# Performance work log

Hardware: AMD Instinct MI355X
Metric: run time of the kernel (lower is better)

The kernel has to match this reference:

```python
import jax, jax.numpy as jnp
import numpy as np

H = 16   # num_attention_heads
G = 4    # num_gqa_groups
D = 64   # head_dim = hidden // H
HIDDEN = 1024
KV_DIM = HIDDEN // H * G  # 256
EPS = 1e-5


def setup_inputs() -> dict:
    key = jax.random.key(0)
    k0, k1, k2, k3 = jax.random.split(key, 4)
    x = jax.random.normal(k0, (8, 4096, HIDDEN), dtype=jnp.float32)
    query_weight = jax.random.normal(k1, (HIDDEN, HIDDEN), dtype=jnp.float32) * 0.02
    key_weight = jax.random.normal(k2, (KV_DIM, HIDDEN), dtype=jnp.float32) * 0.02
    value_weight = jax.random.normal(k3, (KV_DIM, HIDDEN), dtype=jnp.float32) * 0.02
    return {
        "x": x,
        "query_weight": query_weight,
        "key_weight": key_weight,
        "value_weight": value_weight,
        "query_bias": jnp.zeros((HIDDEN,), jnp.float32),
        "key_bias": jnp.zeros((KV_DIM,), jnp.float32),
        "value_bias": jnp.zeros((KV_DIM,), jnp.float32),
        "layer_norm_weight": jnp.ones((HIDDEN,), jnp.float32),
        "layer_norm_bias": jnp.zeros((HIDDEN,), jnp.float32),
    }


def reference(x, query_weight, key_weight, value_weight, query_bias, key_bias,
              value_bias, layer_norm_weight, layer_norm_bias):
    b, s, _ = x.shape
    # Shared LayerNorm (q is k is v path in apply_qkv_norm)
    mu = jnp.mean(x, axis=-1, keepdims=True)
    var = jnp.mean(jnp.square(x - mu), axis=-1, keepdims=True)
    xn = (x - mu) * jax.lax.rsqrt(var + EPS) * layer_norm_weight + layer_norm_bias
    # Q/K/V projections (F.linear: x @ W.T + b)
    q = xn @ query_weight.T + query_bias           # [b, s, H*D]
    k = xn @ key_weight.T + key_bias               # [b, s, G*1*D]
    v = xn @ value_weight.T + value_bias           # [b, s, G*1*D]
    # 'b s (h d) -> b h s d'
    q = q.reshape(b, s, H, D).transpose(0, 2, 1, 3)           # [b, H, s, D]
    # 'b s (g h d) -> b h (g s) d' with h = KV_DIM//(G*D) = 1
    def kv_rearrange(t):
        t = t.reshape(b, s, G, 1, D)                          # b s g h d
        t = t.transpose(0, 3, 2, 1, 4)                        # b h g s d
        return t.reshape(b, 1, G * s, D)                      # [b, 1, G*s, D]
    return q, kv_rearrange(k), kv_rearrange(v)
```

## Files before the change

kernel.cpp:

```cpp
#include <hip/hip_runtime.h>
#include <hip/hip_bf16.h>


#define HIDDEN 1024
#define NTOK   32768

typedef __bf16 bf16x8 __attribute__((ext_vector_type(8)));
typedef float  f32x4  __attribute__((ext_vector_type(4)));

#define GLOBAL_AS(p) ((const __attribute__((address_space(1))) void*)(p))
#define LDS_AS(p)    ((__attribute__((address_space(3))) void*)(p))

__device__ __forceinline__ unsigned short f2bf(float f) {
  union { float f; unsigned int i; } x; x.f = f;
  unsigned int r = x.i + 0x7FFFu + ((x.i >> 16) & 1u);
  return (unsigned short)(r >> 16);
}

__global__ __launch_bounds__(256) void ln_kernel(
    const float* __restrict__ x,
    const float* __restrict__ gamma,
    const float* __restrict__ beta,
    unsigned short* __restrict__ xn) {
  const int row = blockIdx.x;
  const int t   = threadIdx.x;
  const size_t base = (size_t)row * HIDDEN;

  const float4 v = ((const float4*)(x + base))[t];
  float s  = v.x + v.y + v.z + v.w;
  float s2 = v.x*v.x + v.y*v.y + v.z*v.z + v.w*v.w;
#pragma unroll
  for (int off = 32; off >= 1; off >>= 1) {
    s  += __shfl_xor(s,  off);
    s2 += __shfl_xor(s2, off);
  }
  __shared__ float red[8];
  const int w = t >> 6;
  if ((t & 63) == 0) { red[w] = s; red[4 + w] = s2; }
  __syncthreads();
  s  = red[0] + red[1] + red[2] + red[3];
  s2 = red[4] + red[5] + red[6] + red[7];
  const float mu   = s * (1.0f / HIDDEN);
  const float rstd = rsqrtf(s2 * (1.0f / HIDDEN) - mu * mu + 1e-5f);

  const float4 g  = ((const float4*)gamma)[t];
  const float4 bb = ((const float4*)beta)[t];
  ushort4 o;
  o.x = f2bf((v.x - mu) * rstd * g.x + bb.x);
  o.y = f2bf((v.y - mu) * rstd * g.y + bb.y);
  o.z = f2bf((v.z - mu) * rstd * g.z + bb.z);
  o.w = f2bf((v.w - mu) * rstd * g.w + bb.w);
  ((ushort4*)(xn + base))[t] = o;
}

__global__ __launch_bounds__(256) void cvt_kernel(
    const float* __restrict__ src, unsigned short* __restrict__ dst) {
  const int i = blockIdx.x * 256 + threadIdx.x;
  const float4 v = ((const float4*)src)[i];
  ushort4 o;
  o.x = f2bf(v.x); o.y = f2bf(v.y); o.z = f2bf(v.z); o.w = f2bf(v.w);
  ((ushort4*)dst)[i] = o;
}

__global__ __launch_bounds__(512, 2) void qkv_gemm(
    const unsigned short* __restrict__ xn,
    const unsigned short* __restrict__ wq,
    const unsigned short* __restrict__ wk,
    const unsigned short* __restrict__ wv,
    const float* __restrict__ bq,
    const float* __restrict__ bk,
    const float* __restrict__ bv,
    float* __restrict__ out) {
  __shared__ unsigned short Al[4 * 8192];
  __shared__ unsigned short Bl[4 * 8192];

  const int bid = blockIdx.x;
  const int swz = (bid & 7) * 96 + (bid >> 3);
  const int mt  = swz / 6;
  const int nt  = swz % 6;
  const int brow = mt * 256;

  const unsigned short* wbase; const float* biasptr;
  int segcol; size_t obase; int hg;
  if (nt < 4)       { wbase = wq + (size_t)nt * 256 * HIDDEN; biasptr = bq; segcol = nt * 256; obase = 0u;        hg = 16; }
  else if (nt == 4) { wbase = wk;                             biasptr = bk; segcol = 0;        obase = 33554432u; hg = 4;  }
  else              { wbase = wv;                             biasptr = bv; segcol = 0;        obase = 41943040u; hg = 4;  }

  const int t = threadIdx.x;
  const int w = t >> 6, lane = t & 63;
  const int wm = w >> 2, wn = w & 3;
  const int l15 = lane & 15, hi = lane >> 4;

  const int r0 = t >> 2,        c0 = ((t & 3) * 8) ^ (((r0 >> 1) & 3) << 3);
  const int r1 = (512 + t) >> 2, c1 = ((t & 3) * 8) ^ (((r1 >> 1) & 3) << 3);
  const unsigned short* aS0 = xn    + (size_t)(brow + r0) * HIDDEN + c0;
  const unsigned short* aS1 = xn    + (size_t)(brow + r1) * HIDDEN + c1;
  const unsigned short* bS0 = wbase + (size_t)r0 * HIDDEN + c0;
  const unsigned short* bS1 = wbase + (size_t)r1 * HIDDEN + c1;
  const int ldsW = w * 512;

  const int sz   = ((l15 >> 1) & 3) << 3;
  const int aOff0 = (wm * 128 + l15) * 32 + ((hi * 8) ^ sz);
  const int bOff0 = (wn * 64  + l15) * 32 + ((hi * 8) ^ sz);

  f32x4 acc[8][4];
#pragma unroll
  for (int m = 0; m < 8; ++m)
#pragma unroll
    for (int n = 0; n < 4; ++n) acc[m][n] = (f32x4){0.f, 0.f, 0.f, 0.f};

  auto stage = [&](int j) {
    const int bb = (j & 3) * 8192;
    const int kk = j << 5;
    __builtin_amdgcn_global_load_lds(GLOBAL_AS(aS0 + kk), LDS_AS(Al + bb + ldsW),        16, 0, 0);
    __builtin_amdgcn_global_load_lds(GLOBAL_AS(aS1 + kk), LDS_AS(Al + bb + 4096 + ldsW), 16, 0, 0);
    __builtin_amdgcn_global_load_lds(GLOBAL_AS(bS0 + kk), LDS_AS(Bl + bb + ldsW),        16, 0, 0);
    __builtin_amdgcn_global_load_lds(GLOBAL_AS(bS1 + kk), LDS_AS(Bl + bb + 4096 + ldsW), 16, 0, 0);
  };

  auto compute = [&](int j) {
    const unsigned short* Ab = Al + (j & 3) * 8192;
    const unsigned short* Bb = Bl + (j & 3) * 8192;
    bf16x8 bfr[4];
#pragma unroll
    for (int n = 0; n < 4; ++n) bfr[n] = *(const bf16x8*)(Bb + bOff0 + n * 512);
    bf16x8 af[8];
#pragma unroll
    for (int m = 0; m < 8; ++m) af[m] = *(const bf16x8*)(Ab + aOff0 + m * 512);
    __builtin_amdgcn_s_setprio(1);
#pragma unroll
    for (int m = 0; m < 8; ++m)
#pragma unroll
      for (int n = 0; n < 4; ++n)
        acc[m][n] = __builtin_amdgcn_mfma_f32_16x16x32_bf16(af[m], bfr[n], acc[m][n], 0, 0, 0);
    __builtin_amdgcn_s_setprio(0);
  };

#define KSTEP(J, VMN, PF) do {                                        \
    asm volatile("s_waitcnt vmcnt(" #VMN ")" ::: "memory");           \
    __builtin_amdgcn_s_barrier();                                     \
    __builtin_amdgcn_sched_barrier(0);                                \
    if (PF) stage((J) + 3);                                           \
    compute(J);                                                       \
  } while (0)

  stage(0); stage(1); stage(2);
  for (int j = 0; j < 29; ++j) { KSTEP(j, 8, true); }
  KSTEP(29, 8, false);
  KSTEP(30, 4, false);
  KSTEP(31, 0, false);
#undef KSTEP

  const int col_l = l15;
  const int row_l = hi * 4;
#pragma unroll
  for (int n = 0; n < 4; ++n) {
    const int ncolseg = segcol + wn * 64 + n * 16 + col_l;
    const float bias = biasptr[ncolseg];
    const int g = ncolseg >> 6;
    const int d = ncolseg & 63;
#pragma unroll
    for (int m = 0; m < 8; ++m) {
#pragma unroll
      for (int j = 0; j < 4; ++j) {
        const int token = brow + wm * 128 + m * 16 + row_l + j;
        const int b = token >> 12, s = token & 4095;
        const size_t off = obase + (size_t)(b * hg + g) * 262144u + (size_t)s * 64u + d;
        out[off] = acc[m][n][j] + bias;
      }
    }
  }
}

extern "C" void kernel_launch(void* const* d_in, const int* in_sizes, int n_in,
                              void* d_out, int out_size, void* d_ws, size_t ws_size,
                              hipStream_t stream) {
  const float* x  = (const float*)d_in[0];
  const float* wq = (const float*)d_in[1];
  const float* wk = (const float*)d_in[2];
  const float* wv = (const float*)d_in[3];
  const float* bq = (const float*)d_in[4];
  const float* bk = (const float*)d_in[5];
  const float* bv = (const float*)d_in[6];
  const float* g  = (const float*)d_in[7];
  const float* be = (const float*)d_in[8];
  float* out = (float*)d_out;

  unsigned short* xn  = (unsigned short*)d_ws;
  unsigned short* wqb = (unsigned short*)((char*)d_ws + (64u << 20));
  unsigned short* wkb = wqb + 1024 * 1024;
  unsigned short* wvb = wkb + 256 * 1024;

  ln_kernel<<<NTOK, 256, 0, stream>>>(x, g, be, xn);
  cvt_kernel<<<1024, 256, 0, stream>>>(wq, wqb);
  cvt_kernel<<<256,  256, 0, stream>>>(wk, wkb);
  cvt_kernel<<<256,  256, 0, stream>>>(wv, wvb);
  qkv_gemm<<<768, 512, 0, stream>>>(xn, wqb, wkb, wvb, bq, bk, bv, out);
}
```

Before: 198.9 us.

## Restructure GEMM main loop into 8-phase interleaved load/compute ping-pong schedule

Replaces the 4-deep ring of 32-wide K stages with two 64-wide K buffers, each split into two 32-wide halves. Each K-tile is processed in fine-grained phases that interleave LDS fragment reads, global-to-LDS prefetch of the next tiles, and half-width MFMA batches, with barriers between phases. The LDS swizzle and the per-thread staging addressing are also reworked. The aim is better overlap of memory traffic with matrix-core work, at the cost of many more barriers and a more fragile hand-written wait-count schedule.

```diff
diff --git a/kernel.cpp b/kernel.cpp
--- a/kernel.cpp
+++ b/kernel.cpp
@@ -71,8 +71,8 @@
     const float* __restrict__ bk,
     const float* __restrict__ bv,
     float* __restrict__ out) {
-  __shared__ unsigned short Al[4 * 8192];
-  __shared__ unsigned short Bl[4 * 8192];
+  __shared__ unsigned short Alds[32768];
+  __shared__ unsigned short Blds[32768];
 
   const int bid = blockIdx.x;
   const int swz = (bid & 7) * 96 + (bid >> 3);
@@ -91,65 +91,92 @@
   const int wm = w >> 2, wn = w & 3;
   const int l15 = lane & 15, hi = lane >> 4;
 
-  const int r0 = t >> 2,        c0 = ((t & 3) * 8) ^ (((r0 >> 1) & 3) << 3);
-  const int r1 = (512 + t) >> 2, c1 = ((t & 3) * 8) ^ (((r1 >> 1) & 3) << 3);
-  const unsigned short* aS0 = xn    + (size_t)(brow + r0) * HIDDEN + c0;
-  const unsigned short* aS1 = xn    + (size_t)(brow + r1) * HIDDEN + c1;
-  const unsigned short* bS0 = wbase + (size_t)r0 * HIDDEN + c0;
-  const unsigned short* bS1 = wbase + (size_t)r1 * HIDDEN + c1;
-  const int ldsW = w * 512;
-
-  const int sz   = ((l15 >> 1) & 3) << 3;
-  const int aOff0 = (wm * 128 + l15) * 32 + ((hi * 8) ^ sz);
-  const int bOff0 = (wn * 64  + l15) * 32 + ((hi * 8) ^ sz);
+  const int sr  = 2 * w * 16 + (lane >> 2);
+  const int scg = ((lane & 3) ^ ((lane >> 2) & 3)) * 8;
+  const unsigned short* aST = xn    + (size_t)(brow + sr) * HIDDEN + scg;
+  const unsigned short* bST = wbase + (size_t)sr * HIDDEN + scg;
+  const int ldsq = 2 * w * 512;
+
+  const int rdx  = (hi ^ (l15 & 3)) * 8;
+  const int rowA = wm * 128 + l15;
+  const int rowB = wn * 64  + l15;
 
   f32x4 acc[8][4];
 #pragma unroll
   for (int m = 0; m < 8; ++m)
 #pragma unroll
     for (int n = 0; n < 4; ++n) acc[m][n] = (f32x4){0.f, 0.f, 0.f, 0.f};
-
-  auto stage = [&](int j) {
-    const int bb = (j & 3) * 8192;
-    const int kk = j << 5;
-    __builtin_amdgcn_global_load_lds(GLOBAL_AS(aS0 + kk), LDS_AS(Al + bb + ldsW),        16, 0, 0);
-    __builtin_amdgcn_global_load_lds(GLOBAL_AS(aS1 + kk), LDS_AS(Al + bb + 4096 + ldsW), 16, 0, 0);
-    __builtin_amdgcn_global_load_lds(GLOBAL_AS(bS0 + kk), LDS_AS(Bl + bb + ldsW),        16, 0, 0);
-    __builtin_amdgcn_global_load_lds(GLOBAL_AS(bS1 + kk), LDS_AS(Bl + bb + 4096 + ldsW), 16, 0, 0);
-  };
-
-  auto compute = [&](int j) {
-    const unsigned short* Ab = Al + (j & 3) * 8192;
-    const unsigned short* Bb = Bl + (j & 3) * 8192;
-    bf16x8 bfr[4];
-#pragma unroll
-    for (int n = 0; n < 4; ++n) bfr[n] = *(const bf16x8*)(Bb + bOff0 + n * 512);
-    bf16x8 af[8];
-#pragma unroll
-    for (int m = 0; m < 8; ++m) af[m] = *(const bf16x8*)(Ab + aOff0 + m * 512);
-    __builtin_amdgcn_s_setprio(1);
-#pragma unroll
-    for (int m = 0; m < 8; ++m)
-#pragma unroll
-      for (int n = 0; n < 4; ++n)
-        acc[m][n] = __builtin_amdgcn_mfma_f32_16x16x32_bf16(af[m], bfr[n], acc[m][n], 0, 0, 0);
-    __builtin_amdgcn_s_setprio(0);
-  };
-
-#define KSTEP(J, VMN, PF) do {                                        \
-    asm volatile("s_waitcnt vmcnt(" #VMN ")" ::: "memory");           \
-    __builtin_amdgcn_s_barrier();                                     \
-    __builtin_amdgcn_sched_barrier(0);                                \
-    if (PF) stage((J) + 3);                                           \
-    compute(J);                                                       \
-  } while (0)
-
-  stage(0); stage(1); stage(2);
-  for (int j = 0; j < 29; ++j) { KSTEP(j, 8, true); }
-  KSTEP(29, 8, false);
-  KSTEP(30, 4, false);
-  KSTEP(31, 0, false);
-#undef KSTEP
+  bf16x8 a[8], b[2];
+
+#define STA(BUF, KK, KT) do {                                                   \
+    unsigned short* _d = Alds + (BUF) * 16384 + (KK) * 8192 + ldsq;             \
+    const unsigned short* _s = aST + (size_t)((KT) * 64 + (KK) * 32);           \
+    __builtin_amdgcn_global_load_lds(GLOBAL_AS(_s), LDS_AS(_d), 16, 0, 0);      \
+    __builtin_amdgcn_global_load_lds(GLOBAL_AS(_s + 16 * HIDDEN), LDS_AS(_d + 512), 16, 0, 0); \
+  } while (0)
+#define STB(BUF, KK, KT) do {                                                   \
+    unsigned short* _d = Blds + (BUF) * 16384 + (KK) * 8192 + ldsq;             \
+    const unsigned short* _s = bST + (size_t)((KT) * 64 + (KK) * 32);           \
+    __builtin_amdgcn_global_load_lds(GLOBAL_AS(_s), LDS_AS(_d), 16, 0, 0);      \
+    __builtin_amdgcn_global_load_lds(GLOBAL_AS(_s + 16 * HIDDEN), LDS_AS(_d + 512), 16, 0, 0); \
+  } while (0)
+#define DSA(BUF, KK) do { _Pragma("unroll")                                     \
+    for (int m = 0; m < 8; ++m)                                                 \
+      a[m] = *(const bf16x8*)(Alds + (BUF) * 16384 + (KK) * 8192 + (rowA + m * 16) * 32 + rdx); \
+  } while (0)
+#define DSB(BUF, KK, NB) do { _Pragma("unroll")                                 \
+    for (int n = 0; n < 2; ++n)                                                 \
+      b[n] = *(const bf16x8*)(Blds + (BUF) * 16384 + (KK) * 8192 + (rowB + ((NB) + n) * 16) * 32 + rdx); \
+  } while (0)
+#define MM(NB) do {                                                             \
+    __builtin_amdgcn_s_setprio(1);                                              \
+    _Pragma("unroll") for (int m = 0; m < 8; ++m) {                             \
+      acc[m][(NB)]     = __builtin_amdgcn_mfma_f32_16x16x32_bf16(a[m], b[0], acc[m][(NB)], 0, 0, 0);     \
+      acc[m][(NB) + 1] = __builtin_amdgcn_mfma_f32_16x16x32_bf16(a[m], b[1], acc[m][(NB) + 1], 0, 0, 0); \
+    }                                                                           \
+    __builtin_amdgcn_s_setprio(0);                                              \
+  } while (0)
+#define BARS do { __builtin_amdgcn_s_barrier();                                 \
+    asm volatile("s_waitcnt lgkmcnt(0)" ::: "memory");                          \
+    __builtin_amdgcn_sched_barrier(0); } while (0)
+#define ENDB do { __builtin_amdgcn_s_barrier();                                 \
+    __builtin_amdgcn_sched_barrier(0); } while (0)
+#define VMW(N) asm volatile("s_waitcnt vmcnt(" #N ")" ::: "memory")
+
+  STA(0, 0, 0); STB(0, 0, 0); STA(0, 1, 0); STB(0, 1, 0);
+  STA(1, 0, 1); STB(1, 0, 1); STA(1, 1, 1);
+  VMW(10);
+  __builtin_amdgcn_s_barrier();
+  __builtin_amdgcn_sched_barrier(0);
+
+  for (int i = 0; i < 7; ++i) {
+    const int T = 2 * i;
+     DSA(0, 0); DSB(0, 0, 0); STB(1, 1, T + 1); BARS; MM(0);          ENDB;
+     DSB(0, 0, 2);            STA(0, 0, T + 2); BARS; MM(2); VMW(10); ENDB;
+     DSA(0, 1); DSB(0, 1, 0); STB(0, 0, T + 2); BARS; MM(0);          ENDB;
+     DSB(0, 1, 2);            STA(0, 1, T + 2); BARS; MM(2); VMW(10); ENDB;
+     DSA(1, 0); DSB(1, 0, 0); STB(0, 1, T + 2); BARS; MM(0);          ENDB;
+     DSB(1, 0, 2);            STA(1, 0, T + 3); BARS; MM(2); VMW(10); ENDB;
+     DSA(1, 1); DSB(1, 1, 0); STB(1, 0, T + 3); BARS; MM(0);          ENDB;
+     DSB(1, 1, 2);            STA(1, 1, T + 3); BARS; MM(2); VMW(10); ENDB;
+  }
+   DSA(0, 0); DSB(0, 0, 0); STB(1, 1, 15); BARS; MM(0);         ENDB;
+   DSB(0, 0, 2);                           BARS; MM(2); VMW(8); ENDB;
+   DSA(0, 1); DSB(0, 1, 0);                BARS; MM(0);         ENDB;
+   DSB(0, 1, 2);                           BARS; MM(2); VMW(4); ENDB;
+   DSA(1, 0); DSB(1, 0, 0);                BARS; MM(0);         ENDB;
+   DSB(1, 0, 2);                           BARS; MM(2); VMW(0); ENDB;
+   DSA(1, 1); DSB(1, 1, 0);                BARS; MM(0);         ENDB;
+   DSB(1, 1, 2);                           BARS; MM(2);         ENDB;
+
+#undef STA
+#undef STB
+#undef DSA
+#undef DSB
+#undef MM
+#undef BARS
+#undef ENDB
+#undef VMW
 
   const int col_l = l15;
   const int row_l = hi * 4;
@@ -164,8 +191,8 @@
 #pragma unroll
       for (int j = 0; j < 4; ++j) {
         const int token = brow + wm * 128 + m * 16 + row_l + j;
-        const int b = token >> 12, s = token & 4095;
-        const size_t off = obase + (size_t)(b * hg + g) * 262144u + (size_t)s * 64u + d;
+        const int b_ = token >> 12, s = token & 4095;
+        const size_t off = obase + (size_t)(b_ * hg + g) * 262144u + (size_t)s * 64u + d;
         out[off] = acc[m][n][j] + bias;
       }
     }
```

After: 188.1 us. -5.4%, faster.
